# Kernel optimization log

Hardware: AMD Instinct MI355X
Metric: run time of the kernel (lower is better)

Reference implementation:

```python
import jax, jax.numpy as jnp
import numpy as np

NUM_CAMS = 4
E = 256          # embed_dim
H_HEADS = 8      # num_heads
DH = E // H_HEADS
CIN = 64
FF = 4 * E
N_LAYERS = 2
EPS = 1e-5


def _layer_norm(x, g, b):
    mu = jnp.mean(x, axis=-1, keepdims=True)
    var = jnp.mean((x - mu) ** 2, axis=-1, keepdims=True)
    return (x - mu) * jax.lax.rsqrt(var + EPS) * g + b


def setup_inputs() -> dict:
    key = jax.random.key(0)
    ks = jax.random.split(key, 20)
    s = 0.02
    inp = {
        "features": jax.random.normal(ks[0], (NUM_CAMS, 2, CIN, 96, 96), jnp.float32),
        # 1x1 input projection conv
        "Wp": jax.random.normal(ks[1], (E, CIN), jnp.float32) * s,
        "bp": jnp.zeros((E,), jnp.float32),
        # per-layer attention params (stacked over 2 layers)
        "Wqkv": jax.random.normal(ks[2], (N_LAYERS, 3 * E, E), jnp.float32) * s,
        "bqkv": jnp.zeros((N_LAYERS, 3 * E), jnp.float32),
        "Wo": jax.random.normal(ks[3], (N_LAYERS, E, E), jnp.float32) * s,
        "bo": jnp.zeros((N_LAYERS, E), jnp.float32),
        # FFN
        "W1": jax.random.normal(ks[4], (N_LAYERS, FF, E), jnp.float32) * s,
        "b1": jnp.zeros((N_LAYERS, FF), jnp.float32),
        "W2": jax.random.normal(ks[5], (N_LAYERS, E, FF), jnp.float32) * s,
        "b2": jnp.zeros((N_LAYERS, E), jnp.float32),
        # LayerNorms
        "g1": jnp.ones((N_LAYERS, E), jnp.float32),
        "be1": jnp.zeros((N_LAYERS, E), jnp.float32),
        "g2": jnp.ones((N_LAYERS, E), jnp.float32),
        "be2": jnp.zeros((N_LAYERS, E), jnp.float32),
        # 1x1 output conv
        "Wout": jax.random.normal(ks[6], (CIN, E), jnp.float32) * s,
        "bout": jnp.zeros((CIN,), jnp.float32),
    }
    return inp


def reference(features, Wp, bp, Wqkv, bqkv, Wo, bo, W1, b1, W2, b2,
              g1, be1, g2, be2, Wout, bout):
    n_cam, B, Cin, Hh, Ww = features.shape
    # 1x1 conv projection + rearrange to per-pixel sequences: [B*H*W, n_cam, E]
    x = jnp.einsum('nbchw,ec->bhwne', features, Wp) + bp
    x = x.reshape(B * Hh * Ww, n_cam, E)

    scale = 1.0 / jnp.sqrt(jnp.float32(DH))
    for i in range(N_LAYERS):
        # self-attention (post-norm encoder layer, dropout=identity in eval)
        qkv = x @ Wqkv[i].T + bqkv[i]                      # [N, S, 3E]
        q, k, v = jnp.split(qkv, 3, axis=-1)
        q = q.reshape(-1, n_cam, H_HEADS, DH)
        k = k.reshape(-1, n_cam, H_HEADS, DH)
        v = v.reshape(-1, n_cam, H_HEADS, DH)
        scores = jnp.einsum('nqhd,nkhd->nhqk', q, k) * scale
        attn = jax.nn.softmax(scores, axis=-1)
        sa = jnp.einsum('nhqk,nkhd->nqhd', attn, v).reshape(-1, n_cam, E)
        sa = sa @ Wo[i].T + bo[i]
        x = _layer_norm(x + sa, g1[i], be1[i])
        # FFN (ReLU activation, default)
        ff = jax.nn.relu(x @ W1[i].T + b1[i]) @ W2[i].T + b2[i]
        x = _layer_norm(x + ff, g2[i], be2[i])

    # mean over cameras, back to [B, C, H, W] via 1x1 output conv
    fused = x.mean(axis=1).reshape(B, Hh, Ww, E)
    out = jnp.einsum('bhwe,ce->bchw', fused, Wout) + bout[None, :, None, None]
    return out
```

## Files before the change

kernel.cpp:

```cpp
#include <hip/hip_runtime.h>
#include <cstdint>
#include <cstddef>


typedef __bf16 bf16;
typedef __bf16 bf16x8 __attribute__((ext_vector_type(8)));
typedef __bf16 bf16x4 __attribute__((ext_vector_type(4)));
typedef float  f32x4  __attribute__((ext_vector_type(4)));

__device__ __forceinline__ void async_copy16(const void* g, void* l)
{
    __builtin_amdgcn_global_load_lds(
        (__attribute__((address_space(1))) void*)g,
        (__attribute__((address_space(3))) void*)l,
        16, 0, 0);
}

#define WAITV8_BAR() asm volatile("s_waitcnt vmcnt(8)\ns_barrier" ::: "memory")
#define WAITV4_BAR() asm volatile("s_waitcnt vmcnt(4)\ns_barrier" ::: "memory")
#define WAITV0_BAR() asm volatile("s_waitcnt vmcnt(0)\ns_barrier" ::: "memory")
#define WAITL_BAR()  asm volatile("s_waitcnt lgkmcnt(0)\ns_barrier" ::: "memory")

__global__ void pack_all_k(const float* __restrict__ s0, const float* __restrict__ s1,
                           const float* __restrict__ s2, const float* __restrict__ s3,
                           const float* __restrict__ s4,
                           bf16* __restrict__ d0, bf16* __restrict__ d1,
                           bf16* __restrict__ d2, bf16* __restrict__ d3,
                           bf16* __restrict__ d4)
{
    const int i = blockIdx.x * 256 + threadIdx.x;
    if (i < 393216) {
        const int j = i;
        const int l = (j >= 196608) ? 1 : 0;
        const int r = j - l * 196608;
        const int e     = r & 7;
        const int idx16 = r >> 3;
        const int lane  = idx16 & 63;
        const int l16   = lane & 15;
        const int quad  = lane >> 4;
        const int frag  = idx16 >> 6;
        const int ckk   = frag / 48;
        const int nt    = frag - ckk * 48;
        const int kc    = ckk >> 1, kk = ckk & 1;
        const int n     = nt * 16 + l16;
        const int k     = kc * 64 + (kk * 4 + quad) * 8 + e;
        d0[j] = (bf16)s0[l * 196608 + n * 256 + k];
    } else if (i < 524288) {
        const int j = i - 393216;
        const int l = j >> 16, r = j & 65535;
        const int e     = r & 7;
        const int idx16 = r >> 3;
        const int lane  = idx16 & 63;
        const int l16   = lane & 15;
        const int quad  = lane >> 4;
        const int frag  = idx16 >> 6;
        const int s     = frag >> 4, nt = frag & 15;
        const int n     = nt * 16 + l16;
        const int k     = s * 32 + quad * 8 + e;
        d1[j] = (bf16)s1[l * 65536 + n * 256 + k];
    } else if (i < 1048576) {
        const int j = i - 524288;
        const int l = j >> 18, r = j & 262143;
        const int e     = r & 7;
        const int idx16 = r >> 3;
        const int l16   = idx16 & 15;
        const int quad  = (idx16 >> 4) & 3;
        const int nt    = (idx16 >> 6) & 7;
        const int kk    = (idx16 >> 9) & 1;
        const int q     = (idx16 >> 10) & 3;
        const int hc    = idx16 >> 12;
        const int row   = hc * 128 + nt * 16 + l16;
        const int k     = q * 64 + (kk * 4 + quad) * 8 + e;
        d2[j] = (bf16)s2[l * 262144 + row * 256 + k];
    } else if (i < 1572864) {
        const int j = i - 1048576;
        const int l = j >> 18, r = j & 262143;
        const int e     = r & 7;
        const int idx16 = r >> 3;
        const int l16   = idx16 & 15;
        const int quad  = (idx16 >> 4) & 3;
        const int nt    = (idx16 >> 6) & 15;
        const int q     = (idx16 >> 10) & 3;
        const int hc    = idx16 >> 12;
        const int n     = nt * 16 + l16;
        const int k     = hc * 128 + q * 32 + quad * 8 + e;
        d3[j] = (bf16)s3[l * 262144 + n * 1024 + k];
    }
    else                  d4[i - 1572864] = (bf16)s4[i - 1572864];
}

__global__ __launch_bounds__(256) void feat_pack_k(const float* __restrict__ feat,
                                                   bf16* __restrict__ Xf)
{
    __shared__ float ft[64][68];

    const int tid  = threadIdx.x;
    const int camb = blockIdx.y;
    const int cam  = camb >> 1;
    const int b    = camb & 1;
    const int hw0  = blockIdx.x * 64;

    const float* fb = feat + (size_t)camb * 64 * 9216 + hw0;
#pragma unroll
    for (int rep = 0; rep < 16; ++rep) {
        const int idx = rep * 256 + tid;
        const int c = idx >> 6, p = idx & 63;
        ft[p][c] = fb[(size_t)c * 9216 + p];
    }
    __syncthreads();

    const int pbase = b * 9216 + hw0;
#pragma unroll
    for (int rep = 0; rep < 2; ++rep) {
        const int idx = rep * 256 + tid;
        const int p = idx >> 3, cc = idx & 7;
        const f32x4 a = *(const f32x4*)(&ft[p][cc * 8]);
        const f32x4 c4 = *(const f32x4*)(&ft[p][cc * 8 + 4]);
        bf16x8 v;
#pragma unroll
        for (int i = 0; i < 4; ++i) { v[i] = (bf16)a[i]; v[4 + i] = (bf16)c4[i]; }
        const size_t t = (size_t)(pbase + p) * 4 + cam;
        *(bf16x8*)(Xf + t * 64 + cc * 8) = v;
    }
}

template <bool RELU>
__global__ __launch_bounds__(256, 2) void gemm_bt(
    const bf16* __restrict__ A, const bf16* __restrict__ B,
    const float* __restrict__ bias, bf16* __restrict__ C,
    int N, int K)
{
    __shared__ __align__(16) char smem[65536];

    const int tid  = threadIdx.x;
    const int lane = tid & 63;
    const int wv   = tid >> 6;
    const int wm   = wv >> 1;
    const int wn   = wv & 1;
    const int bm   = blockIdx.y * 128;
    const int bn   = blockIdx.x * 128;

    const int r8  = lane >> 3;
    const int p8  = lane & 7;
    const int gch = p8 ^ r8;

    const int quad = lane >> 4;
    const int l16  = lane & 15;

    f32x4 acc[4][4] = {};
    const int nk = K >> 6;

    auto STAGE = [&](int kc, char* base) {
#pragma unroll
        for (int inst = 0; inst < 4; ++inst) {
            const int row = wv * 32 + inst * 8 + r8;
            async_copy16(A + (size_t)(bm + row) * K + (kc * 64 + gch * 8),
                         base + (wv * 4 + inst) * 1024);
            async_copy16(B + (size_t)(bn + row) * K + (kc * 64 + gch * 8),
                         base + 16384 + (wv * 4 + inst) * 1024);
        }
    };

    STAGE(0, smem);

#pragma unroll 1
    for (int kc = 0; kc < nk; ++kc) {
        const char* cur = smem + (size_t)(kc & 1) * 32768;
        if (kc + 1 < nk) {
            STAGE(kc + 1, smem + (size_t)((kc + 1) & 1) * 32768);
            WAITV8_BAR();
        } else {
            WAITV0_BAR();
        }

#pragma unroll
        for (int kk = 0; kk < 2; ++kk) {
            bf16x8 af[4], bfr[4];
            const int lch = kk * 4 + quad;
#pragma unroll
            for (int i = 0; i < 4; ++i) {
                const int m = wm * 64 + i * 16 + l16;
                af[i] = *(const bf16x8*)(cur + (m * 8 + (lch ^ (m & 7))) * 16);
                const int n = wn * 64 + i * 16 + l16;
                bfr[i] = *(const bf16x8*)(cur + 16384 + (n * 8 + (lch ^ (n & 7))) * 16);
            }
            __builtin_amdgcn_s_setprio(1);
#pragma unroll
            for (int i = 0; i < 4; ++i)
#pragma unroll
                for (int j = 0; j < 4; ++j)
                    acc[i][j] = __builtin_amdgcn_mfma_f32_16x16x32_bf16(
                        af[i], bfr[j], acc[i][j], 0, 0, 0);
            __builtin_amdgcn_s_setprio(0);
        }
        WAITL_BAR();
    }

#pragma unroll
    for (int j = 0; j < 4; ++j) {
        const int n = bn + wn * 64 + j * 16 + l16;
        const float bv = bias[n];
#pragma unroll
        for (int i = 0; i < 4; ++i) {
            const int mb = bm + wm * 64 + i * 16 + quad * 4;
#pragma unroll
            for (int r = 0; r < 4; ++r) {
                float v = acc[i][j][r] + bv;
                if (RELU) v = fmaxf(v, 0.f);
                C[(size_t)(mb + r) * N + n] = (bf16)v;
            }
        }
    }
}

__global__ __launch_bounds__(256, 3) void gemm_qkv_k(
    const bf16* __restrict__ A, const bf16* __restrict__ BP,
    const float* __restrict__ bias, bf16* __restrict__ C)
{
    __shared__ __align__(16) char smem[32768];

    const int tid  = threadIdx.x;
    const int lane = tid & 63;
    const int wv   = tid >> 6;
    const int wn   = wv;
    const int bm   = blockIdx.y * 128;
    const int bn   = blockIdx.x * 128;
    const int ntb  = blockIdx.x * 8;

    const int r8  = lane >> 3;
    const int p8  = lane & 7;
    const int gch = p8 ^ r8;
    const int quad = lane >> 4;
    const int l16  = lane & 15;

    f32x4 acc[8][2] = {};

    auto STAGE = [&](int kc, char* base) {
#pragma unroll
        for (int inst = 0; inst < 4; ++inst) {
            const int row = wv * 32 + inst * 8 + r8;
            async_copy16(A + (size_t)(bm + row) * 256 + (kc * 64 + gch * 8),
                         base + (wv * 4 + inst) * 1024);
        }
    };

    STAGE(0, smem);

#pragma unroll
    for (int kc = 0; kc < 4; ++kc) {
        const char* cur = smem + (size_t)(kc & 1) * 16384;
        if (kc < 3) {
            STAGE(kc + 1, smem + (size_t)((kc + 1) & 1) * 16384);
            WAITV4_BAR();
        } else {
            WAITV0_BAR();
        }

#pragma unroll
        for (int kk = 0; kk < 2; ++kk) {
            const int lch = kk * 4 + quad;
            bf16x8 af[8], bfr[2];
#pragma unroll
            for (int j = 0; j < 2; ++j)
                bfr[j] = *(const bf16x8*)(BP +
                    ((size_t)((kc * 2 + kk) * 48 + ntb + wn * 2 + j)) * 512
                    + lane * 8);
#pragma unroll
            for (int i = 0; i < 8; ++i) {
                const int m = i * 16 + l16;
                af[i] = *(const bf16x8*)(cur + (m * 8 + (lch ^ (m & 7))) * 16);
            }
            __builtin_amdgcn_s_setprio(1);
#pragma unroll
            for (int i = 0; i < 8; ++i)
#pragma unroll
                for (int j = 0; j < 2; ++j)
                    acc[i][j] = __builtin_amdgcn_mfma_f32_16x16x32_bf16(
                        af[i], bfr[j], acc[i][j], 0, 0, 0);
            __builtin_amdgcn_s_setprio(0);
        }
        WAITL_BAR();
    }

#pragma unroll
    for (int j = 0; j < 2; ++j) {
        const int n = bn + wn * 32 + j * 16 + l16;
        const float bv = bias[n];
#pragma unroll
        for (int i = 0; i < 8; ++i) {
            const int mb = bm + i * 16 + quad * 4;
#pragma unroll
            for (int r = 0; r < 4; ++r)
                C[(size_t)(mb + r) * 768 + n] = (bf16)(acc[i][j][r] + bv);
        }
    }
}

__global__ __launch_bounds__(256, 3) void attn_ln_k(
    const bf16* __restrict__ QKV, const bf16* __restrict__ WoP,
    const float* __restrict__ bias, const bf16* __restrict__ Xres,
    const float* __restrict__ gam, const float* __restrict__ bet,
    bf16* __restrict__ Xout)
{
    __shared__ __align__(16) char smem[34816];
    bf16* SAs = (bf16*)smem;
    float2 (*red)[4] = (float2 (*)[4])(void*)(smem + 32768);

    const int tid  = threadIdx.x;
    const int lane = tid & 63;
    const int wv   = tid >> 6;
    const int wn   = wv;
    const int quad = lane >> 4;
    const int l16  = lane & 15;
    const int bm   = blockIdx.x * 64;
    const int rot  = (blockIdx.x >> 3) & 7;

    {
        const int hh = lane >> 3;
        const int cg = lane & 7;
        const int s0 = blockIdx.x * 16;
        const float SCALE = 0.17677669529663687f;

#pragma unroll
        for (int g = 0; g < 4; ++g) {
            const int seq = s0 + g * 4 + wv;
            const bf16* bse = QKV + (size_t)seq * 3072 + hh * 32 + cg * 4;

            float qf[4][4], kf[4][4], vf[4][4];
#pragma unroll
            for (int i = 0; i < 4; ++i) {
                const bf16x4 qb = *(const bf16x4*)(bse + i * 768);
                const bf16x4 kb = *(const bf16x4*)(bse + i * 768 + 256);
                const bf16x4 vb = *(const bf16x4*)(bse + i * 768 + 512);
#pragma unroll
                for (int d = 0; d < 4; ++d) {
                    qf[i][d] = (float)qb[d];
                    kf[i][d] = (float)kb[d];
                    vf[i][d] = (float)vb[d];
                }
            }

            float sc[4][4];
#pragma unroll
            for (int i = 0; i < 4; ++i)
#pragma unroll
                for (int j = 0; j < 4; ++j)
                    sc[i][j] = qf[i][0] * kf[j][0] + qf[i][1] * kf[j][1]
                             + qf[i][2] * kf[j][2] + qf[i][3] * kf[j][3];

#pragma unroll
            for (int msk = 1; msk <= 4; msk <<= 1)
#pragma unroll
                for (int i = 0; i < 4; ++i)
#pragma unroll
                    for (int j = 0; j < 4; ++j)
                        sc[i][j] += __shfl_xor(sc[i][j], msk, 64);

#pragma unroll
            for (int i = 0; i < 4; ++i) {
                const float v0 = sc[i][0] * SCALE, v1 = sc[i][1] * SCALE;
                const float v2 = sc[i][2] * SCALE, v3 = sc[i][3] * SCALE;
                const float mx = fmaxf(fmaxf(v0, v1), fmaxf(v2, v3));
                const float e0 = expf(v0 - mx), e1 = expf(v1 - mx);
                const float e2 = expf(v2 - mx), e3 = expf(v3 - mx);
                const float inv = 1.f / (e0 + e1 + e2 + e3);
                sc[i][0] = e0 * inv; sc[i][1] = e1 * inv;
                sc[i][2] = e2 * inv; sc[i][3] = e3 * inv;
            }

#pragma unroll
            for (int i = 0; i < 4; ++i) {
                bf16x4 ov;
#pragma unroll
                for (int d = 0; d < 4; ++d) {
                    const float o = sc[i][0] * vf[0][d] + sc[i][1] * vf[1][d]
                                  + sc[i][2] * vf[2][d] + sc[i][3] * vf[3][d];
                    ov[d] = (bf16)o;
                }
                const int m  = (g * 4 + wv) * 4 + i;
                const int gc = lane >> 1;
                const int sl = (gc & 24) | ((gc ^ m) & 7);
                *(bf16x4*)((char*)SAs + (m * 32 + sl) * 16 + (lane & 1) * 8) = ov;
            }
        }
    }
    __syncthreads();

    f32x4 acc[4][4] = {};

#pragma unroll
    for (int s = 0; s < 8; ++s) {
        const int sr = (s + rot) & 7;
        const int gc = sr * 4 + quad;
        bf16x8 af[4], bfr[4];
#pragma unroll
        for (int j = 0; j < 4; ++j)
            bfr[j] = *(const bf16x8*)(WoP +
                ((size_t)(sr * 16 + wn * 4 + j)) * 512 + lane * 8);
#pragma unroll
        for (int i = 0; i < 4; ++i) {
            const int m  = i * 16 + l16;
            const int sl = (gc & 24) | ((gc ^ m) & 7);
            af[i] = *(const bf16x8*)((const char*)SAs + (m * 32 + sl) * 16);
        }
        __builtin_amdgcn_s_setprio(1);
#pragma unroll
        for (int i = 0; i < 4; ++i)
#pragma unroll
            for (int j = 0; j < 4; ++j)
                acc[i][j] = __builtin_amdgcn_mfma_f32_16x16x32_bf16(
                    af[i], bfr[j], acc[i][j], 0, 0, 0);
        __builtin_amdgcn_s_setprio(0);
    }

    float bv[4], gv[4], bev[4];
#pragma unroll
    for (int j = 0; j < 4; ++j) {
        const int n = wn * 64 + j * 16 + l16;
        bv[j] = bias[n]; gv[j] = gam[n]; bev[j] = bet[n];
    }

#pragma unroll
    for (int i = 0; i < 4; ++i) {
#pragma unroll
        for (int r = 0; r < 4; ++r) {
            const int rl = i * 16 + quad * 4 + r;
            const size_t row = (size_t)(bm + rl);
            float s1 = 0.f, s2 = 0.f;
#pragma unroll
            for (int j = 0; j < 4; ++j) {
                const int n = wn * 64 + j * 16 + l16;
                const float v = acc[i][j][r] + bv[j] + (float)Xres[row * 256 + n];
                acc[i][j][r] = v;
                s1 += v; s2 += v * v;
            }
#pragma unroll
            for (int off = 1; off < 16; off <<= 1) {
                s1 += __shfl_xor(s1, off, 64);
                s2 += __shfl_xor(s2, off, 64);
            }
            if (l16 == 0) red[rl][wn] = make_float2(s1, s2);
        }
    }
    __syncthreads();

#pragma unroll
    for (int i = 0; i < 4; ++i) {
#pragma unroll
        for (int r = 0; r < 4; ++r) {
            const int rl = i * 16 + quad * 4 + r;
            const float2 p0 = red[rl][0], p1 = red[rl][1];
            const float2 p2 = red[rl][2], p3 = red[rl][3];
            const float mu  = (p0.x + p1.x + p2.x + p3.x) * (1.f / 256.f);
            const float ex2 = (p0.y + p1.y + p2.y + p3.y) * (1.f / 256.f);
            const float rstd = rsqrtf(fmaxf(ex2 - mu * mu, 0.f) + 1e-5f);
            const size_t row = (size_t)(bm + rl);
#pragma unroll
            for (int j = 0; j < 4; ++j) {
                const int n = wn * 64 + j * 16 + l16;
                Xout[row * 256 + n] = (bf16)((acc[i][j][r] - mu) * rstd * gv[j] + bev[j]);
            }
        }
    }
}

__global__ __launch_bounds__(256, 3) void ffn_fused_k(
    const bf16* __restrict__ X,
    const bf16* __restrict__ W1P, const float* __restrict__ b1,
    const bf16* __restrict__ W2P, const float* __restrict__ b2,
    const float* __restrict__ gam, const float* __restrict__ bet,
    bf16* __restrict__ Xout)
{
    __shared__ __align__(16) char smem[49152];
    bf16* Xs = (bf16*)smem;
    bf16* Ts = (bf16*)(smem + 32768);
    float2 (*red)[4] = (float2 (*)[4])(void*)(smem + 32768);

    const int tid  = threadIdx.x;
    const int lane = tid & 63;
    const int wn   = tid >> 6;
    const int quad = lane >> 4;
    const int l16  = lane & 15;
    const int bm   = blockIdx.x * 64;
    const int rot  = (blockIdx.x >> 3) & 7;
    const int rot2 = (blockIdx.x >> 6) & 3;

#pragma unroll
    for (int it = 0; it < 8; ++it) {
        const int L = it * 256 + tid;
        const int row = L >> 5, slot = L & 31;
        const int gch = (slot & 24) | ((slot ^ row) & 7);
        async_copy16(X + (size_t)(bm + row) * 256 + gch * 8,
                     (char*)Xs + (size_t)L * 16);
    }
    WAITV0_BAR();

    f32x4 acc2[4][4] = {};

#pragma unroll 1
    for (int hc = 0; hc < 8; ++hc) {
        const int hcr = (hc + rot) & 7;
        float b1v[2];
#pragma unroll
        for (int j = 0; j < 2; ++j)
            b1v[j] = b1[hcr * 128 + wn * 32 + j * 16 + l16];

        f32x4 accA[4][2] = {};

#pragma unroll
        for (int q0 = 0; q0 < 4; ++q0) {
            const int q = (q0 + rot2) & 3;
#pragma unroll
            for (int kk = 0; kk < 2; ++kk) {
                const int ch = kk * 4 + quad;
                const int gc = q * 8 + ch;
                bf16x8 af[4], bfr[2];
#pragma unroll
                for (int j = 0; j < 2; ++j)
                    bfr[j] = *(const bf16x8*)(W1P +
                        ((size_t)(((hcr * 4 + q) * 2 + kk) * 8) + wn * 2 + j) * 512
                        + lane * 8);
#pragma unroll
                for (int i = 0; i < 4; ++i) {
                    const int m  = i * 16 + l16;
                    const int sl = (gc & 24) | ((gc ^ m) & 7);
                    af[i] = *(const bf16x8*)((const char*)Xs + (m * 32 + sl) * 16);
                }
                __builtin_amdgcn_s_setprio(1);
#pragma unroll
                for (int i = 0; i < 4; ++i)
#pragma unroll
                    for (int j = 0; j < 2; ++j)
                        accA[i][j] = __builtin_amdgcn_mfma_f32_16x16x32_bf16(
                            af[i], bfr[j], accA[i][j], 0, 0, 0);
                __builtin_amdgcn_s_setprio(0);
            }
        }

#pragma unroll
        for (int j = 0; j < 2; ++j) {
            const int h  = wn * 32 + j * 16 + l16;
            const float bb = b1v[j];
            const int g  = h >> 3;
#pragma unroll
            for (int i = 0; i < 4; ++i)
#pragma unroll
                for (int r = 0; r < 4; ++r) {
                    const int m  = i * 16 + quad * 4 + r;
                    const int sl = (g & 8) | ((g ^ m) & 7);
                    const float v = fmaxf(accA[i][j][r] + bb, 0.f);
                    *((bf16*)((char*)Ts + (m * 16 + sl) * 16 + (h & 7) * 2)) = (bf16)v;
                }
        }
        WAITL_BAR();

#pragma unroll
        for (int q0 = 0; q0 < 4; ++q0) {
            const int q = (q0 + rot2) & 3;
            const int tc = q * 4 + quad;
            bf16x8 af[4], bfr[4];
#pragma unroll
            for (int j = 0; j < 4; ++j)
                bfr[j] = *(const bf16x8*)(W2P +
                    ((size_t)((hcr * 4 + q) * 16) + wn * 4 + j) * 512
                    + lane * 8);
#pragma unroll
            for (int i = 0; i < 4; ++i) {
                const int m  = i * 16 + l16;
                const int sl = (tc & 8) | ((tc ^ m) & 7);
                af[i] = *(const bf16x8*)((const char*)Ts + (m * 16 + sl) * 16);
            }
            __builtin_amdgcn_s_setprio(1);
#pragma unroll
            for (int i = 0; i < 4; ++i)
#pragma unroll
                for (int j = 0; j < 4; ++j)
                    acc2[i][j] = __builtin_amdgcn_mfma_f32_16x16x32_bf16(
                        af[i], bfr[j], acc2[i][j], 0, 0, 0);
            __builtin_amdgcn_s_setprio(0);
        }
        WAITL_BAR();
    }

    float bv[4], gv[4], bev[4];
#pragma unroll
    for (int j = 0; j < 4; ++j) {
        const int n = wn * 64 + j * 16 + l16;
        bv[j] = b2[n]; gv[j] = gam[n]; bev[j] = bet[n];
    }

#pragma unroll
    for (int i = 0; i < 4; ++i) {
#pragma unroll
        for (int r = 0; r < 4; ++r) {
            const int rl = i * 16 + quad * 4 + r;
            float s1 = 0.f, s2 = 0.f;
#pragma unroll
            for (int j = 0; j < 4; ++j) {
                const int n  = wn * 64 + j * 16 + l16;
                const int gc = n >> 3;
                const int sl = (gc & 24) | ((gc ^ rl) & 7);
                const float xr = (float)*((const bf16*)((const char*)Xs +
                                   (rl * 32 + sl) * 16 + (n & 7) * 2));
                const float v = acc2[i][j][r] + bv[j] + xr;
                acc2[i][j][r] = v;
                s1 += v; s2 += v * v;
            }
#pragma unroll
            for (int off = 1; off < 16; off <<= 1) {
                s1 += __shfl_xor(s1, off, 64);
                s2 += __shfl_xor(s2, off, 64);
            }
            if (l16 == 0) red[rl][wn] = make_float2(s1, s2);
        }
    }
    __syncthreads();

#pragma unroll
    for (int i = 0; i < 4; ++i) {
#pragma unroll
        for (int r = 0; r < 4; ++r) {
            const int rl = i * 16 + quad * 4 + r;
            const float2 p0 = red[rl][0], p1 = red[rl][1];
            const float2 p2 = red[rl][2], p3 = red[rl][3];
            const float mu  = (p0.x + p1.x + p2.x + p3.x) * (1.f / 256.f);
            const float ex2 = (p0.y + p1.y + p2.y + p3.y) * (1.f / 256.f);
            const float rstd = rsqrtf(fmaxf(ex2 - mu * mu, 0.f) + 1e-5f);
            const size_t row = (size_t)(bm + rl);
#pragma unroll
            for (int j = 0; j < 4; ++j) {
                const int n = wn * 64 + j * 16 + l16;
                Xout[row * 256 + n] = (bf16)((acc2[i][j][r] - mu) * rstd * gv[j] + bev[j]);
            }
        }
    }
}

__global__ __launch_bounds__(256) void out_proj_k(const bf16* __restrict__ X,
                                                  const float* __restrict__ Wout,
                                                  const float* __restrict__ bout,
                                                  float* __restrict__ out)
{
    __shared__ float fused[16][260];
    const int tid = threadIdx.x;
    const int p0  = blockIdx.x * 16;

#pragma unroll
    for (int it = 0; it < 16; ++it) {
        const int idx = it * 256 + tid;
        const int pix = idx >> 8, e = idx & 255;
        const size_t base = (size_t)(p0 + pix) * 1024 + e;
        const float s = (float)X[base] + (float)X[base + 256] +
                        (float)X[base + 512] + (float)X[base + 768];
        fused[pix][e] = s * 0.25f;
    }
    __syncthreads();

    const int pix = tid & 15;
    const int c0  = tid >> 4;
    const int p   = p0 + pix;
    const int b   = p / 9216;
    const int hw  = p % 9216;
#pragma unroll
    for (int it = 0; it < 4; ++it) {
        const int c = it * 16 + c0;
        const float* w = Wout + c * 256;
        float acc = bout[c];
#pragma unroll 8
        for (int e = 0; e < 256; ++e) acc += fused[pix][e] * w[e];
        out[((size_t)b * 64 + c) * 9216 + hw] = acc;
    }
}

extern "C" void kernel_launch(void* const* d_in, const int* in_sizes, int n_in,
                              void* d_out, int out_size, void* d_ws, size_t ws_size,
                              hipStream_t stream)
{
    const float* features = (const float*)d_in[0];
    const float* Wp   = (const float*)d_in[1];
    const float* bp   = (const float*)d_in[2];
    const float* Wqkv = (const float*)d_in[3];
    const float* bqkv = (const float*)d_in[4];
    const float* Wo   = (const float*)d_in[5];
    const float* bo   = (const float*)d_in[6];
    const float* W1   = (const float*)d_in[7];
    const float* b1   = (const float*)d_in[8];
    const float* W2   = (const float*)d_in[9];
    const float* b2   = (const float*)d_in[10];
    const float* g1   = (const float*)d_in[11];
    const float* be1  = (const float*)d_in[12];
    const float* g2   = (const float*)d_in[13];
    const float* be2  = (const float*)d_in[14];
    const float* Wout = (const float*)d_in[15];
    const float* bout = (const float*)d_in[16];
    float* out = (float*)d_out;

    char* ws = (char*)d_ws;
    bf16* X   = (bf16*)(ws);
    bf16* QKV = (bf16*)(ws + 37748736ull);
    bf16* Xf  = (bf16*)(ws + 188743680ull);
    bf16* WpB = (bf16*)(ws + 198180864ull);
    bf16* Wb  = (bf16*)(ws + 226492416ull);

    bf16* WqkvB = Wb;
    bf16* WoB   = Wb + 393216;
    bf16* W1B   = Wb + 524288;
    bf16* W2B   = Wb + 1048576;

    pack_all_k<<<6208, 256, 0, stream>>>(Wqkv, Wo, W1, W2, Wp,
                                         WqkvB, WoB, W1B, W2B, WpB);

    feat_pack_k<<<dim3(144, 8), 256, 0, stream>>>(features, Xf);
    gemm_bt<false><<<dim3(2, 576), 256, 0, stream>>>(Xf, WpB, bp, X, 256, 64);

    for (int l = 0; l < 2; ++l) {
        gemm_qkv_k<<<dim3(6, 576), 256, 0, stream>>>(
            X, WqkvB + l * 196608, bqkv + l * 768, QKV);
        attn_ln_k<<<1152, 256, 0, stream>>>(
            QKV, WoB + l * 65536, bo + l * 256, X,
            g1 + l * 256, be1 + l * 256, X);
        ffn_fused_k<<<1152, 256, 0, stream>>>(
            X, W1B + l * 262144, b1 + l * 1024,
            W2B + l * 262144, b2 + l * 256,
            g2 + l * 256, be2 + l * 256, X);
    }

    out_proj_k<<<1152, 256, 0, stream>>>(X, Wout, bout, out);
}
```

Measured before the change: 572.0 us.

## Load full A row-tile once in QKV GEMM and loop over all N tiles

The QKV GEMM now has each block stage its whole 128x256 A tile in LDS once (64KB), then loop over all six 128-wide output column tiles, reading weights from global memory. Before, six blocks each re-read the same A rows through a double-buffered K pipeline. A per-block rotation of the starting column tile is meant to spread weight reads. The change lowers occupancy (launch bounds 2, larger LDS) and drops the overlap of loads with compute. It also removes the rot2 quarter rotation in the FFN kernel.

```diff
diff --git a/kernel.cpp b/kernel.cpp
--- a/kernel.cpp
+++ b/kernel.cpp
@@ -213,85 +213,75 @@
     }
 }
 
-__global__ __launch_bounds__(256, 3) void gemm_qkv_k(
+__global__ __launch_bounds__(256, 2) void gemm_qkv_k(
     const bf16* __restrict__ A, const bf16* __restrict__ BP,
     const float* __restrict__ bias, bf16* __restrict__ C)
 {
-    __shared__ __align__(16) char smem[32768];
+    __shared__ __align__(16) char smem[65536];
 
     const int tid  = threadIdx.x;
     const int lane = tid & 63;
-    const int wv   = tid >> 6;
-    const int wn   = wv;
-    const int bm   = blockIdx.y * 128;
-    const int bn   = blockIdx.x * 128;
-    const int ntb  = blockIdx.x * 8;
-
-    const int r8  = lane >> 3;
-    const int p8  = lane & 7;
-    const int gch = p8 ^ r8;
+    const int wn   = tid >> 6;
+    const int bm   = blockIdx.x * 128;
     const int quad = lane >> 4;
     const int l16  = lane & 15;
-
-    f32x4 acc[8][2] = {};
-
-    auto STAGE = [&](int kc, char* base) {
-#pragma unroll
-        for (int inst = 0; inst < 4; ++inst) {
-            const int row = wv * 32 + inst * 8 + r8;
-            async_copy16(A + (size_t)(bm + row) * 256 + (kc * 64 + gch * 8),
-                         base + (wv * 4 + inst) * 1024);
-        }
-    };
-
-    STAGE(0, smem);
-
-#pragma unroll
-    for (int kc = 0; kc < 4; ++kc) {
-        const char* cur = smem + (size_t)(kc & 1) * 16384;
-        if (kc < 3) {
-            STAGE(kc + 1, smem + (size_t)((kc + 1) & 1) * 16384);
-            WAITV4_BAR();
-        } else {
-            WAITV0_BAR();
-        }
-
-#pragma unroll
-        for (int kk = 0; kk < 2; ++kk) {
-            const int lch = kk * 4 + quad;
-            bf16x8 af[8], bfr[2];
-#pragma unroll
-            for (int j = 0; j < 2; ++j)
-                bfr[j] = *(const bf16x8*)(BP +
-                    ((size_t)((kc * 2 + kk) * 48 + ntb + wn * 2 + j)) * 512
-                    + lane * 8);
+    const int prot = (int)((blockIdx.x >> 3) % 6);
+
+#pragma unroll
+    for (int it = 0; it < 16; ++it) {
+        const int L = it * 256 + tid;
+        const int row = L >> 5, slot = L & 31;
+        const int gch = (slot & 24) | ((slot ^ row) & 7);
+        async_copy16(A + (size_t)(bm + row) * 256 + gch * 8,
+                     (char*)smem + (size_t)L * 16);
+    }
+    WAITV0_BAR();
+
+#pragma unroll 1
+    for (int p0 = 0; p0 < 6; ++p0) {
+        int p = p0 + prot; if (p >= 6) p -= 6;
+        f32x4 acc[8][2] = {};
+
+#pragma unroll
+        for (int kc = 0; kc < 4; ++kc) {
+#pragma unroll
+            for (int kk = 0; kk < 2; ++kk) {
+                const int lch = kk * 4 + quad;
+                bf16x8 af[8], bfr[2];
+#pragma unroll
+                for (int j = 0; j < 2; ++j)
+                    bfr[j] = *(const bf16x8*)(BP +
+                        ((size_t)((kc * 2 + kk) * 48 + p * 8 + wn * 2 + j)) * 512
+                        + lane * 8);
+#pragma unroll
+                for (int i = 0; i < 8; ++i) {
+                    const int m  = i * 16 + l16;
+                    const int gc = kc * 8 + lch;
+                    const int sl = (gc & 24) | ((gc ^ m) & 7);
+                    af[i] = *(const bf16x8*)((const char*)smem + (m * 32 + sl) * 16);
+                }
+                __builtin_amdgcn_s_setprio(1);
+#pragma unroll
+                for (int i = 0; i < 8; ++i)
+#pragma unroll
+                    for (int j = 0; j < 2; ++j)
+                        acc[i][j] = __builtin_amdgcn_mfma_f32_16x16x32_bf16(
+                            af[i], bfr[j], acc[i][j], 0, 0, 0);
+                __builtin_amdgcn_s_setprio(0);
+            }
+        }
+
+#pragma unroll
+        for (int j = 0; j < 2; ++j) {
+            const int n = p * 128 + wn * 32 + j * 16 + l16;
+            const float bv = bias[n];
 #pragma unroll
             for (int i = 0; i < 8; ++i) {
-                const int m = i * 16 + l16;
-                af[i] = *(const bf16x8*)(cur + (m * 8 + (lch ^ (m & 7))) * 16);
-            }
-            __builtin_amdgcn_s_setprio(1);
-#pragma unroll
-            for (int i = 0; i < 8; ++i)
-#pragma unroll
-                for (int j = 0; j < 2; ++j)
-                    acc[i][j] = __builtin_amdgcn_mfma_f32_16x16x32_bf16(
-                        af[i], bfr[j], acc[i][j], 0, 0, 0);
-            __builtin_amdgcn_s_setprio(0);
-        }
-        WAITL_BAR();
-    }
-
-#pragma unroll
-    for (int j = 0; j < 2; ++j) {
-        const int n = bn + wn * 32 + j * 16 + l16;
-        const float bv = bias[n];
-#pragma unroll
-        for (int i = 0; i < 8; ++i) {
-            const int mb = bm + i * 16 + quad * 4;
-#pragma unroll
-            for (int r = 0; r < 4; ++r)
-                C[(size_t)(mb + r) * 768 + n] = (bf16)(acc[i][j][r] + bv);
+                const int mb = bm + i * 16 + quad * 4;
+#pragma unroll
+                for (int r = 0; r < 4; ++r)
+                    C[(size_t)(mb + r) * 768 + n] = (bf16)(acc[i][j][r] + bv);
+            }
         }
     }
 }
@@ -483,7 +473,6 @@
     const int l16  = lane & 15;
     const int bm   = blockIdx.x * 64;
     const int rot  = (blockIdx.x >> 3) & 7;
-    const int rot2 = (blockIdx.x >> 6) & 3;
 
 #pragma unroll
     for (int it = 0; it < 8; ++it) {
@@ -508,8 +497,7 @@
         f32x4 accA[4][2] = {};
 
 #pragma unroll
-        for (int q0 = 0; q0 < 4; ++q0) {
-            const int q = (q0 + rot2) & 3;
+        for (int q = 0; q < 4; ++q) {
 #pragma unroll
             for (int kk = 0; kk < 2; ++kk) {
                 const int ch = kk * 4 + quad;
@@ -555,8 +543,7 @@
         WAITL_BAR();
 
 #pragma unroll
-        for (int q0 = 0; q0 < 4; ++q0) {
-            const int q = (q0 + rot2) & 3;
+        for (int q = 0; q < 4; ++q) {
             const int tc = q * 4 + quad;
             bf16x8 af[4], bfr[4];
 #pragma unroll
@@ -714,7 +701,7 @@
     gemm_bt<false><<<dim3(2, 576), 256, 0, stream>>>(Xf, WpB, bp, X, 256, 64);
 
     for (int l = 0; l < 2; ++l) {
-        gemm_qkv_k<<<dim3(6, 576), 256, 0, stream>>>(
+        gemm_qkv_k<<<576, 256, 0, stream>>>(
             X, WqkvB + l * 196608, bqkv + l * 768, QKV);
         attn_ln_k<<<1152, 256, 0, stream>>>(
             QKV, WoB + l * 65536, bo + l * 256, X,
```

After: 913.3 us. 1.6x slower.
